# Optimization experiments

Hardware: AMD Instinct MI355X
Metric: run time of the kernel (lower is better)

## Reference

```python
import jax, jax.numpy as jnp
import numpy as np

B, S, HID = 2, 2048, 2048
H, HKV, D = 16, 8, 128
CHUNK = 512
THETA = 1000000.0
NEG = -1e9


def setup_inputs() -> dict:
    key = jax.random.key(0)
    ks = jax.random.split(key, 10)
    hidden_states = jax.random.normal(ks[0], (B, S, HID), dtype=jnp.float32)
    # additive causal mask (0 on/below diagonal, -1e9 above)
    tri = jnp.tril(jnp.ones((S, S), dtype=bool))
    attention_mask = jnp.where(tri, 0.0, NEG).astype(jnp.float32)
    attention_mask = jnp.broadcast_to(attention_mask[None, None], (B, 1, S, S))
    w = 0.02
    Wq = jax.random.normal(ks[1], (HID, H * D), dtype=jnp.float32) * w
    bq = jax.random.normal(ks[2], (H * D,), dtype=jnp.float32) * w
    Wk = jax.random.normal(ks[3], (HID, HKV * D), dtype=jnp.float32) * w
    bk = jax.random.normal(ks[4], (HKV * D,), dtype=jnp.float32) * w
    Wv = jax.random.normal(ks[5], (HID, HKV * D), dtype=jnp.float32) * w
    bv = jax.random.normal(ks[6], (HKV * D,), dtype=jnp.float32) * w
    Wo = jax.random.normal(ks[7], (H * D, HID), dtype=jnp.float32) * w
    bo = jax.random.normal(ks[8], (HID,), dtype=jnp.float32) * w
    return {"hidden_states": hidden_states, "attention_mask": attention_mask,
            "Wq": Wq, "bq": bq, "Wk": Wk, "bk": bk, "Wv": Wv, "bv": bv,
            "Wo": Wo, "bo": bo}


def _rope_tables(seq_len, dim):
    inv_freq = 1.0 / (THETA ** (jnp.arange(0, dim, 2, dtype=jnp.float32) / dim))
    pos = jnp.arange(seq_len, dtype=jnp.float32)
    freqs = pos[:, None] * inv_freq[None, :]          # [S, D/2]
    emb = jnp.concatenate([freqs, freqs], axis=-1)    # [S, D]
    return jnp.cos(emb)[None, None], jnp.sin(emb)[None, None]  # [1,1,S,D]


def _rotate_half(x):
    x1, x2 = jnp.split(x, 2, axis=-1)
    return jnp.concatenate([-x2, x1], axis=-1)


def _attn_forward(hidden_states, attention_mask, Wq, bq, Wk, bk, Wv, bv, Wo, bo):
    bsz, s, _ = hidden_states.shape
    q = (hidden_states @ Wq + bq).reshape(bsz, s, H, D).transpose(0, 2, 1, 3)
    k = (hidden_states @ Wk + bk).reshape(bsz, s, HKV, D).transpose(0, 2, 1, 3)
    v = (hidden_states @ Wv + bv).reshape(bsz, s, HKV, D).transpose(0, 2, 1, 3)
    cos, sin = _rope_tables(s, D)
    q = q * cos + _rotate_half(q) * sin
    k = k * cos + _rotate_half(k) * sin
    n_rep = H // HKV
    k = jnp.repeat(k, n_rep, axis=1)  # repeat_kv
    v = jnp.repeat(v, n_rep, axis=1)
    scale = 1.0 / jnp.sqrt(jnp.float32(D))
    nq, nk = s // CHUNK, s // CHUNK
    Qc = q.reshape(bsz, H, nq, CHUNK, D)
    Kc = jnp.moveaxis(k.reshape(bsz, H, nk, CHUNK, D), 2, 0)   # [nk,B,H,Ck,D]
    Vc = jnp.moveaxis(v.reshape(bsz, H, nk, CHUNK, D), 2, 0)
    Mc = jnp.moveaxis(attention_mask.reshape(bsz, 1, nq, CHUNK, nk, CHUNK), 4, 0)  # [nk,B,1,nq,Cq,Ck]

    def step(carry, xs):
        o, m, d = carry
        k_seg, v_seg, m_seg = xs
        # scores: [B,H,nq,Cq,Ck]
        sc = jnp.einsum('bhqcd,bhkd->bhqck', Qc, k_seg) * scale + m_seg
        new_m = jnp.maximum(m, sc.max(axis=-1, keepdims=True))
        e = jnp.exp(sc - new_m)
        sums = e.sum(axis=-1, keepdims=True)
        prev = jnp.exp(m - new_m)          # NOTE: uses running max, as in source
        d_new = prev + sums
        o = (o * prev + jnp.einsum('bhqck,bhkd->bhqcd', e, v_seg)) / d_new
        return (o, new_m, d_new), None

    o0 = jnp.zeros((bsz, H, nq, CHUNK, D), dtype=jnp.float32)
    m0 = jnp.full((bsz, H, nq, CHUNK, 1), -jnp.inf, dtype=jnp.float32)
    d0 = jnp.ones((bsz, H, nq, CHUNK, 1), dtype=jnp.float32)
    (o, m, d), _ = jax.lax.scan(step, (o0, m0, d0), (Kc, Vc, Mc))
    # final rescale: attn_output * exp(max - logsumexp) == o / d_last (source math)
    o = o / d
    attn = o.reshape(bsz, H, s, D).transpose(0, 2, 1, 3).reshape(bsz, s, H * D)
    return attn @ Wo + bo


def reference(hidden_states, attention_mask, Wq, bq, Wk, bk, Wv, bv, Wo, bo):
    return _attn_forward(hidden_states, attention_mask, Wq, bq, Wk, bk, Wv, bv, Wo, bo)
```

## Files before the change

### kernel.cpp

```cpp
#include <hip/hip_runtime.h>
#include <hip/hip_bf16.h>


typedef __attribute__((ext_vector_type(8))) short s8v;
typedef __attribute__((ext_vector_type(4))) float f4v;

#define MFMA16(a, b, c) __builtin_amdgcn_mfma_f32_16x16x32_bf16((a), (b), (c), 0, 0, 0)

typedef unsigned short u16;
typedef const __attribute__((address_space(1))) unsigned int* gas_p;
typedef __attribute__((address_space(3))) unsigned int* las_p;

__device__ __forceinline__ void gl_lds16(const void* g, void* l) {
    __builtin_amdgcn_global_load_lds((gas_p)g, (las_p)l, 16, 0, 0);
}

__device__ __forceinline__ u16 f2b(float f) {
    __hip_bfloat16 h = __float2bfloat16(f);
    return *reinterpret_cast<u16*>(&h);
}
__device__ __forceinline__ float b2f(u16 u) {
    __hip_bfloat16 h;
    *reinterpret_cast<u16*>(&h) = u;
    return __bfloat162float(h);
}

__device__ const unsigned char qt_tab[80] = {
    8, 9, 10, 11, 12, 13, 14, 15,
    16, 16, 17, 17, 18, 18, 19, 19, 20, 20, 21, 21, 22, 22, 23, 23,
    24, 24, 24, 25, 25, 25, 26, 26, 26, 27, 27, 27,
    28, 28, 28, 29, 29, 29, 30, 30, 30, 31, 31, 31,
    31, 23, 15, 7, 30, 22, 14, 6, 29, 21, 13, 5, 28, 20, 12, 4,
    27, 19, 11, 3, 26, 18, 10, 2, 25, 17, 9, 1, 24, 16, 8, 0};
__device__ const unsigned char c_tab[80] = {
    0, 0, 0, 0, 0, 0, 0, 0,
    0, 1, 0, 1, 0, 1, 0, 1, 0, 1, 0, 1, 0, 1, 0, 1,
    0, 1, 2, 0, 1, 2, 0, 1, 2, 0, 1, 2,
    0, 1, 2, 0, 1, 2, 0, 1, 2, 0, 1, 2,
    3, 2, 1, 0, 3, 2, 1, 0, 3, 2, 1, 0, 3, 2, 1, 0,
    3, 2, 1, 0, 3, 2, 1, 0, 3, 2, 1, 0, 3, 2, 1, 0};

__device__ __forceinline__ int uoff(int qt, int c) {
    int qc = qt >> 3;
    if (c < qc) {
        if (qt < 16) return qt - 8;
        if (qt < 24) return 8 + ((qt - 16) << 1) + c;
        return 24 + (qt - 24) * 3 + c;
    }
    return 48 + ((7 - (qt & 7)) << 2) + (3 - qc);
}

__global__ __launch_bounds__(256) void k_cast_hs(const float* __restrict__ src,
                                                 u16* __restrict__ dst) {
    int i = blockIdx.x * 256 + threadIdx.x;
    float4 v = reinterpret_cast<const float4*>(src)[i];
    alignas(8) u16 t[4] = {f2b(v.x), f2b(v.y), f2b(v.z), f2b(v.w)};
    reinterpret_cast<uint2*>(dst)[i] = *reinterpret_cast<uint2*>(t);
}

__global__ __launch_bounds__(256) void k_transpose_w(
    const float* __restrict__ Wq, const float* __restrict__ Wk,
    const float* __restrict__ Wv, const float* __restrict__ Wo,
    u16* __restrict__ wt_all, u16* __restrict__ wo_t) {
    int id = blockIdx.x;
    const float* W; u16* dst; int N, nbase;
    if (id < 4096)      { W = Wq; dst = wt_all; N = 2048; nbase = 0; }
    else if (id < 6144) { W = Wk; dst = wt_all; N = 1024; nbase = 2048; id -= 4096; }
    else if (id < 8192) { W = Wv; dst = wt_all; N = 1024; nbase = 3072; id -= 6144; }
    else                { W = Wo; dst = wo_t;  N = 2048; nbase = 0;    id -= 8192; }
    int tiles_n = N >> 5;
    int k0 = (id / tiles_n) << 5, n0 = (id % tiles_n) << 5;
    __shared__ float t[32][33];
    int tid = threadIdx.x, c = tid & 31, rr = tid >> 5;
#pragma unroll
    for (int i = 0; i < 4; i++) {
        int kk = rr + i * 8;
        t[kk][c] = W[(size_t)(k0 + kk) * N + n0 + c];
    }
    __syncthreads();
#pragma unroll
    for (int i = 0; i < 4; i++) {
        int n = rr + i * 8;
        dst[(size_t)(nbase + n0 + n) * 2048 + k0 + c] = f2b(t[c][n]);
    }
}

__global__ __launch_bounds__(256) void k_bias(const float* __restrict__ bq,
                                              const float* __restrict__ bk,
                                              const float* __restrict__ bv,
                                              float* __restrict__ dst) {
    int i = blockIdx.x * 256 + threadIdx.x;
    float v = (i < 2048) ? bq[i] : (i < 3072) ? bk[i - 2048] : bv[i - 3072];
    dst[i] = v;
}

__global__ __launch_bounds__(256) void k_gemm(
    const u16* __restrict__ A, const u16* __restrict__ Bt,
    const float* __restrict__ bias, void* __restrict__ out,
    int M, int N, int K, int out_f32) {
    __shared__ alignas(16) u16 As[128][32];
    __shared__ alignas(16) u16 Bs[128][32];
    int tid = threadIdx.x;
    int wave = tid >> 6, lane = tid & 63, quad = lane >> 4, l16 = lane & 15;
    int m0 = blockIdx.y << 7, n0 = blockIdx.x << 7;
    int wm = (wave >> 1) << 6, wn = (wave & 1) << 6;
    f4v zero = {0.f, 0.f, 0.f, 0.f};
    f4v acc[4][4];
#pragma unroll
    for (int a = 0; a < 4; a++)
#pragma unroll
        for (int b = 0; b < 4; b++) acc[a][b] = zero;
    int r0 = tid >> 2;
    int gsw = (tid & 3) ^ ((r0 >> 1) & 3);
    const u16* gA = A + (size_t)(m0 + r0) * K + (gsw << 3);
    const u16* gB = Bt + (size_t)(n0 + r0) * K + (gsw << 3);
    int rg = (quad ^ ((l16 >> 1) & 3)) << 3;
    for (int k0 = 0; k0 < K; k0 += 32) {
        __syncthreads();
#pragma unroll
        for (int i = 0; i < 2; i++) {
            gl_lds16(gA + (size_t)(i << 6) * K + k0, (char*)As + (i << 12) + tid * 16);
            gl_lds16(gB + (size_t)(i << 6) * K + k0, (char*)Bs + (i << 12) + tid * 16);
        }
        __syncthreads();
        s8v af[4], bf_[4];
#pragma unroll
        for (int mi = 0; mi < 4; mi++)
            af[mi] = *reinterpret_cast<const s8v*>(&As[wm + mi * 16 + l16][rg]);
#pragma unroll
        for (int ni = 0; ni < 4; ni++)
            bf_[ni] = *reinterpret_cast<const s8v*>(&Bs[wn + ni * 16 + l16][rg]);
#pragma unroll
        for (int mi = 0; mi < 4; mi++)
#pragma unroll
            for (int ni = 0; ni < 4; ni++)
                acc[mi][ni] = MFMA16(af[mi], bf_[ni], acc[mi][ni]);
    }
#pragma unroll
    for (int mi = 0; mi < 4; mi++) {
#pragma unroll
        for (int ni = 0; ni < 4; ni++) {
            int n = n0 + wn + ni * 16 + l16;
            float bsv = bias[n];
#pragma unroll
            for (int r = 0; r < 4; r++) {
                int m = m0 + wm + mi * 16 + (quad << 2) + r;
                float v = acc[mi][ni][r] + bsv;
                if (out_f32)
                    reinterpret_cast<float*>(out)[(size_t)m * N + n] = v;
                else
                    reinterpret_cast<u16*>(out)[(size_t)m * N + n] = f2b(v);
            }
        }
    }
}

__global__ __launch_bounds__(256) void k_rope(const u16* __restrict__ qkv,
                                              u16* __restrict__ qr,
                                              u16* __restrict__ kr) {
    const float qscale = 0.08838834764831845f * 1.44269504088896340f;
    int row = blockIdx.x;
    int b = row >> 11, s = row & 2047;
    const u16* src = qkv + (size_t)row * 4096;
    __shared__ float lcs[64], lsn[64];
    int tid = threadIdx.x;
    if (tid < 64) {
        float fr = (float)s * exp2f((float)tid * -0.31143075889569023f);
        lcs[tid] = cosf(fr);
        lsn[tid] = sinf(fr);
    }
    __syncthreads();
    for (int u = tid; u < 1536; u += 256) {
        int hh, i;
        const u16* sp;
        u16* dp;
        float sc;
        if (u < 1024) {
            hh = u >> 6; i = u & 63;
            sp = src + hh * 128;
            dp = qr + ((size_t)(b * 16 + hh) * 2048 + s) * 128;
            sc = qscale;
        } else {
            int u2 = u - 1024;
            hh = u2 >> 6; i = u2 & 63;
            sp = src + 2048 + hh * 128;
            dp = kr + ((size_t)(b * 8 + hh) * 2048 + s) * 128;
            sc = 1.f;
        }
        float x1 = b2f(sp[i]);
        float x2 = b2f(sp[i + 64]);
        float cs = lcs[i], sn = lsn[i];
        dp[i]      = f2b((x1 * cs - x2 * sn) * sc);
        dp[i + 64] = f2b((x2 * cs + x1 * sn) * sc);
    }
}

__global__ __launch_bounds__(256) void k_vtrans(const u16* __restrict__ qkv,
                                                u16* __restrict__ vt) {
    int bkv = blockIdx.z, b = bkv >> 3, kv = bkv & 7;
    int s0 = blockIdx.x << 6, d0 = blockIdx.y << 5;
    __shared__ alignas(16) u16 t[32][72];
    int tid = threadIdx.x, c = tid & 31, rr = tid >> 5;
#pragma unroll
    for (int i = 0; i < 8; i++) {
        int s = s0 + rr + i * 8;
        t[c][rr + i * 8] = qkv[(size_t)(b * 2048 + s) * 4096 + 3072 + kv * 128 + d0 + c];
    }
    __syncthreads();
    int dd = tid >> 3, sc8 = (tid & 7) << 3;
    *reinterpret_cast<uint4*>(&vt[((size_t)(b * 8 + kv) * 128 + d0 + dd) * 2048 + s0 + sc8]) =
        *reinterpret_cast<const uint4*>(&t[dd][sc8]);
}

__global__ __launch_bounds__(256) void k_attn_part(const u16* __restrict__ qr,
                                                   const u16* __restrict__ kr,
                                                   const u16* __restrict__ vt,
                                                   u16* __restrict__ PVp,
                                                   float* __restrict__ scp) {
    const float NINF = -__builtin_inff();
    __shared__ alignas(16) u16 Ks[2][64 * 128];
    __shared__ alignas(16) u16 Vs[2][128 * 64];
    __shared__ alignas(16) u16 Pb[4][16][40];

    int tid = threadIdx.x;
    int wv = tid >> 6, lane = tid & 63, quad = lane >> 4, l16 = lane & 15;
    int x = blockIdx.x, h = blockIdx.y, b = blockIdx.z, kvh = h >> 1;
    int qt = qt_tab[x], c = c_tab[x], qc = qt >> 3;
    int nt = (c < qc) ? 8 : (qt & 7) + 1;
    int diagT = (c == qc) ? (qt & 7) : 8;
    int kbase = c << 9;
    const u16* Qp = qr + ((size_t)(b * 16 + h) * 2048 + qt * 64 + wv * 16) * 128;
    const u16* Kp = kr + ((size_t)(b * 8 + kvh) * 2048) * 128;
    const u16* Vp = vt + ((size_t)(b * 8 + kvh) * 128) * 2048;

    s8v qf[4];
#pragma unroll
    for (int sl = 0; sl < 4; sl++)
        qf[sl] = *reinterpret_cast<const s8v*>(&Qp[l16 * 128 + sl * 32 + (quad << 3)]);
    s8v ones;
#pragma unroll
    for (int i = 0; i < 8; i++) ones[i] = (short)0x3F80;

    int krow = tid >> 4, kg = (tid & 15) ^ krow;
    int vd = tid >> 3, vg = (tid & 7) ^ (vd & 7);
    auto stage = [&](int t) {
        int kbt = kbase + (t << 6);
        const u16* kgp = Kp + (size_t)(kbt + krow) * 128 + (kg << 3);
        const u16* vgp = Vp + (size_t)vd * 2048 + kbt + (vg << 3);
        char* kd = (char*)&Ks[t & 1][0];
        char* vdst = (char*)&Vs[t & 1][0];
#pragma unroll
        for (int i = 0; i < 4; i++) {
            gl_lds16(kgp + (size_t)(i << 4) * 128, kd + (i << 12) + tid * 16);
            gl_lds16(vgp + (size_t)(i << 5) * 2048, vdst + (i << 12) + tid * 16);
        }
    };

    f4v zero = {0.f, 0.f, 0.f, 0.f};
    f4v u[8], sums = zero;
#pragma unroll
    for (int ni = 0; ni < 8; ni++) u[ni] = zero;
    float tmx[4] = {NINF, NINF, NINF, NINF};

    stage(0);
    for (int t = 0; t < nt; t++) {
        __syncthreads();
        if (t + 1 < nt) stage(t + 1);
        const char* Kbuf = (const char*)&Ks[t & 1][0];
        const char* Vbuf = (const char*)&Vs[t & 1][0];

        int subs = (t == diagT) ? (wv + 1) : 4;
        int ns2 = (subs + 1) >> 1;
#pragma unroll
        for (int s2 = 0; s2 < 2; s2++) {
            if (s2 >= ns2) continue;
#pragma unroll
            for (int half = 0; half < 2; half++) {
                int sub = (s2 << 1) + half;
                if (sub >= subs) {
#pragma unroll
                    for (int r = 0; r < 4; r++)
                        Pb[wv][(quad << 2) + r][(half << 4) + l16] = (u16)0;
                    continue;
                }
                f4v s = zero;
#pragma unroll
                for (int sl = 0; sl < 4; sl++) {
                    s8v kf = *reinterpret_cast<const s8v*>(
                        Kbuf + ((sub << 4) + l16) * 256 + ((((sl << 2) + quad) ^ l16) << 4));
                    s = MFMA16(qf[sl], kf, s);
                }
                bool part = (t == diagT) && (sub == wv);
#pragma unroll
                for (int r = 0; r < 4; r++) {
                    float v = s[r];
                    if (part && (l16 > (quad << 2) + r)) v = NINF;
                    tmx[r] = fmaxf(tmx[r], v);
                    float e = __builtin_amdgcn_exp2f(v);
                    Pb[wv][(quad << 2) + r][(half << 4) + l16] = f2b(e);
                }
            }
            s8v pf = *reinterpret_cast<const s8v*>(&Pb[wv][l16][quad << 3]);
            sums = MFMA16(pf, ones, sums);
#pragma unroll
            for (int ni = 0; ni < 8; ni++) {
                s8v vf = *reinterpret_cast<const s8v*>(
                    Vbuf + ((ni << 4) + l16) * 128 + ((((s2 << 2) + quad) ^ (l16 & 7)) << 4));
                u[ni] = MFMA16(pf, vf, u[ni]);
            }
        }
    }
#pragma unroll
    for (int r = 0; r < 4; r++)
#pragma unroll
        for (int off = 1; off < 16; off <<= 1)
            tmx[r] = fmaxf(tmx[r], __shfl_xor(tmx[r], off));
    float resc[4];
#pragma unroll
    for (int r = 0; r < 4; r++) resc[r] = __builtin_amdgcn_exp2f(-tmx[r]);

    int slot = (b * 16 + h) * 80 + x;
    u16* pvdst = PVp + (size_t)slot * 8192;
#pragma unroll
    for (int ni = 0; ni < 8; ni++)
#pragma unroll
        for (int r = 0; r < 4; r++)
            pvdst[(wv * 16 + (quad << 2) + r) * 128 + ni * 16 + l16] =
                f2b(u[ni][r] * resc[r]);
    if (l16 == 0) {
        float* scd = scp + (size_t)slot * 128 + wv * 16 + (quad << 2);
#pragma unroll
        for (int r = 0; r < 4; r++) {
            scd[r] = tmx[r] * 0.6931471805599453f;
            scd[64 + r] = sums[r] * resc[r];
        }
    }
}

__global__ __launch_bounds__(256) void k_attn_comb(const u16* __restrict__ PVp,
                                                   const float* __restrict__ scp,
                                                   u16* __restrict__ attnb) {
    int qt = blockIdx.x, h = blockIdx.y, b = blockIdx.z, qc = qt >> 3;
    int tid = threadIdx.x, row = tid >> 2, d0 = (tid & 3) << 5;
    int bh = b * 16 + h;
    float o[32];
#pragma unroll
    for (int i = 0; i < 32; i++) o[i] = 0.f;
    float mprev = -__builtin_inff(), dlast = 1.f;
    for (int cc = 0; cc <= qc; cc++) {
        int slot = bh * 80 + uoff(qt, cc);
        float ch = scp[(size_t)slot * 128 + row];
        float sh = scp[(size_t)slot * 128 + 64 + row];
        float mnew = fmaxf(mprev, ch);
        float p = __expf(mprev - mnew);
        float lam = __expf(ch - mnew);
        float dd = p + lam * sh;
        float inv = 1.f / dd;
        const u16* pv = PVp + (size_t)slot * 8192 + row * 128 + d0;
#pragma unroll
        for (int k = 0; k < 4; k++) {
            s8v v8 = *reinterpret_cast<const s8v*>(pv + (k << 3));
#pragma unroll
            for (int j = 0; j < 8; j++) {
                int i = (k << 3) + j;
                o[i] = (o[i] * p + lam * b2f((u16)v8[j])) * inv;
            }
        }
        mprev = mnew;
        dlast = dd;
    }
    if (qc == 3) {
        float inv = 1.f / dlast;
#pragma unroll
        for (int i = 0; i < 32; i++) o[i] *= inv;
    }
    alignas(16) u16 ob[32];
#pragma unroll
    for (int i = 0; i < 32; i++) ob[i] = f2b(o[i]);
    u16* dst = attnb + (size_t)(b * 2048 + qt * 64 + row) * 2048 + h * 128 + d0;
#pragma unroll
    for (int k = 0; k < 4; k++)
        reinterpret_cast<uint4*>(dst)[k] = reinterpret_cast<const uint4*>(ob)[k];
}

extern "C" void kernel_launch(void* const* d_in, const int* in_sizes, int n_in,
                              void* d_out, int out_size, void* d_ws, size_t ws_size,
                              hipStream_t stream) {
    (void)in_sizes; (void)n_in; (void)out_size; (void)ws_size;
    const float* hs = (const float*)d_in[0];
    const float* Wq = (const float*)d_in[2];
    const float* bq = (const float*)d_in[3];
    const float* Wk = (const float*)d_in[4];
    const float* bk = (const float*)d_in[5];
    const float* Wv = (const float*)d_in[6];
    const float* bv = (const float*)d_in[7];
    const float* Wo = (const float*)d_in[8];
    const float* bo = (const float*)d_in[9];

    char* ws = (char*)d_ws;
    u16* hsb      = (u16*)(ws);
    u16* qr       = hsb;
    u16* attnb    = hsb;
    u16* wt_all   = (u16*)(ws + (16u << 20));
    u16* kr       = wt_all;
    u16* vt       = (u16*)(ws + (24u << 20));
    u16* wo_t     = (u16*)(ws + (32u << 20));
    float* bias_c = (float*)(ws + (40u << 20));
    u16* qkv      = (u16*)(ws + (40u << 20) + 65536);
    u16* PVp      = qkv;
    float* scp    = (float*)(ws + (40u << 20) + 65536 + 41943040u);

    k_cast_hs<<<8192, 256, 0, stream>>>(hs, hsb);
    k_transpose_w<<<12288, 256, 0, stream>>>(Wq, Wk, Wv, Wo, wt_all, wo_t);
    k_bias<<<16, 256, 0, stream>>>(bq, bk, bv, bias_c);
    k_gemm<<<dim3(32, 32), 256, 0, stream>>>(hsb, wt_all, bias_c, qkv,
                                             4096, 4096, 2048, 0);
    k_rope<<<4096, 256, 0, stream>>>(qkv, qr, kr);
    k_vtrans<<<dim3(32, 4, 16), 256, 0, stream>>>(qkv, vt);
    k_attn_part<<<dim3(80, 16, 2), 256, 0, stream>>>(qr, kr, vt, PVp, scp);
    k_attn_comb<<<dim3(32, 16, 2), 256, 0, stream>>>(PVp, scp, attnb);
    k_gemm<<<dim3(16, 32), 256, 0, stream>>>(attnb, wo_t, bo, d_out,
                                             4096, 2048, 2048, 1);
}
```

Baseline: 430.9 us.

## Double attention query tile per wave, deepen GEMM K-step, vectorize weight transpose

```diff
diff --git a/kernel.cpp b/kernel.cpp
--- a/kernel.cpp
+++ b/kernel.cpp
@@ -25,29 +25,25 @@
     return __bfloat162float(h);
 }
 
-__device__ const unsigned char qt_tab[80] = {
-    8, 9, 10, 11, 12, 13, 14, 15,
-    16, 16, 17, 17, 18, 18, 19, 19, 20, 20, 21, 21, 22, 22, 23, 23,
-    24, 24, 24, 25, 25, 25, 26, 26, 26, 27, 27, 27,
-    28, 28, 28, 29, 29, 29, 30, 30, 30, 31, 31, 31,
-    31, 23, 15, 7, 30, 22, 14, 6, 29, 21, 13, 5, 28, 20, 12, 4,
-    27, 19, 11, 3, 26, 18, 10, 2, 25, 17, 9, 1, 24, 16, 8, 0};
-__device__ const unsigned char c_tab[80] = {
-    0, 0, 0, 0, 0, 0, 0, 0,
-    0, 1, 0, 1, 0, 1, 0, 1, 0, 1, 0, 1, 0, 1, 0, 1,
+__device__ const unsigned char qt_tab[40] = {
+    4, 5, 6, 7,
+    8, 8, 9, 9, 10, 10, 11, 11,
+    12, 12, 12, 13, 13, 13, 14, 14, 14, 15, 15, 15,
+    3, 7, 11, 15, 2, 6, 10, 14, 1, 5, 9, 13, 0, 4, 8, 12};
+__device__ const unsigned char c_tab[40] = {
+    0, 0, 0, 0,
+    0, 1, 0, 1, 0, 1, 0, 1,
     0, 1, 2, 0, 1, 2, 0, 1, 2, 0, 1, 2,
-    0, 1, 2, 0, 1, 2, 0, 1, 2, 0, 1, 2,
-    3, 2, 1, 0, 3, 2, 1, 0, 3, 2, 1, 0, 3, 2, 1, 0,
-    3, 2, 1, 0, 3, 2, 1, 0, 3, 2, 1, 0, 3, 2, 1, 0};
-
-__device__ __forceinline__ int uoff(int qt, int c) {
-    int qc = qt >> 3;
+    0, 1, 2, 3, 0, 1, 2, 3, 0, 1, 2, 3, 0, 1, 2, 3};
+
+__device__ __forceinline__ int uoff40(int qt, int c) {
+    int qc = qt >> 2;
     if (c < qc) {
-        if (qt < 16) return qt - 8;
-        if (qt < 24) return 8 + ((qt - 16) << 1) + c;
-        return 24 + (qt - 24) * 3 + c;
-    }
-    return 48 + ((7 - (qt & 7)) << 2) + (3 - qc);
+        if (qt < 8) return qt - 4;
+        if (qt < 12) return 4 + ((qt - 8) << 1) + c;
+        return 12 + (qt - 12) * 3 + c;
+    }
+    return 24 + ((3 - (qt & 3)) << 2) + qc;
 }
 
 __global__ __launch_bounds__(256) void k_cast_hs(const float* __restrict__ src,
@@ -71,17 +67,21 @@
     int tiles_n = N >> 5;
     int k0 = (id / tiles_n) << 5, n0 = (id % tiles_n) << 5;
     __shared__ float t[32][33];
-    int tid = threadIdx.x, c = tid & 31, rr = tid >> 5;
-#pragma unroll
-    for (int i = 0; i < 4; i++) {
-        int kk = rr + i * 8;
-        t[kk][c] = W[(size_t)(k0 + kk) * N + n0 + c];
+    int tid = threadIdx.x;
+    {
+        int row = tid >> 3, c4 = (tid & 7) << 2;
+        float4 v = *reinterpret_cast<const float4*>(&W[(size_t)(k0 + row) * N + n0 + c4]);
+        t[row][c4 + 0] = v.x; t[row][c4 + 1] = v.y;
+        t[row][c4 + 2] = v.z; t[row][c4 + 3] = v.w;
     }
     __syncthreads();
-#pragma unroll
-    for (int i = 0; i < 4; i++) {
-        int n = rr + i * 8;
-        dst[(size_t)(nbase + n0 + n) * 2048 + k0 + c] = f2b(t[c][n]);
+    {
+        int n = tid >> 3, kq = (tid & 7) << 2;
+        alignas(8) u16 p[4];
+#pragma unroll
+        for (int j = 0; j < 4; j++) p[j] = f2b(t[kq + j][n]);
+        *reinterpret_cast<uint2*>(&dst[(size_t)(nbase + n0 + n) * 2048 + k0 + kq]) =
+            *reinterpret_cast<uint2*>(p);
     }
 }
 
@@ -98,8 +98,8 @@
     const u16* __restrict__ A, const u16* __restrict__ Bt,
     const float* __restrict__ bias, void* __restrict__ out,
     int M, int N, int K, int out_f32) {
-    __shared__ alignas(16) u16 As[128][32];
-    __shared__ alignas(16) u16 Bs[128][32];
+    __shared__ alignas(16) u16 As[128][64];
+    __shared__ alignas(16) u16 Bs[128][64];
     int tid = threadIdx.x;
     int wave = tid >> 6, lane = tid & 63, quad = lane >> 4, l16 = lane & 15;
     int m0 = blockIdx.y << 7, n0 = blockIdx.x << 7;
@@ -110,31 +110,34 @@
     for (int a = 0; a < 4; a++)
 #pragma unroll
         for (int b = 0; b < 4; b++) acc[a][b] = zero;
-    int r0 = tid >> 2;
-    int gsw = (tid & 3) ^ ((r0 >> 1) & 3);
+    int r0 = tid >> 3;
+    int gsw = (tid & 7) ^ (r0 & 7);
     const u16* gA = A + (size_t)(m0 + r0) * K + (gsw << 3);
     const u16* gB = Bt + (size_t)(n0 + r0) * K + (gsw << 3);
-    int rg = (quad ^ ((l16 >> 1) & 3)) << 3;
-    for (int k0 = 0; k0 < K; k0 += 32) {
+    for (int k0 = 0; k0 < K; k0 += 64) {
         __syncthreads();
 #pragma unroll
-        for (int i = 0; i < 2; i++) {
-            gl_lds16(gA + (size_t)(i << 6) * K + k0, (char*)As + (i << 12) + tid * 16);
-            gl_lds16(gB + (size_t)(i << 6) * K + k0, (char*)Bs + (i << 12) + tid * 16);
+        for (int i = 0; i < 4; i++) {
+            gl_lds16(gA + (size_t)(i << 5) * K + k0, (char*)As + (i << 12) + tid * 16);
+            gl_lds16(gB + (size_t)(i << 5) * K + k0, (char*)Bs + (i << 12) + tid * 16);
         }
         __syncthreads();
-        s8v af[4], bf_[4];
-#pragma unroll
-        for (int mi = 0; mi < 4; mi++)
-            af[mi] = *reinterpret_cast<const s8v*>(&As[wm + mi * 16 + l16][rg]);
-#pragma unroll
-        for (int ni = 0; ni < 4; ni++)
-            bf_[ni] = *reinterpret_cast<const s8v*>(&Bs[wn + ni * 16 + l16][rg]);
-#pragma unroll
-        for (int mi = 0; mi < 4; mi++)
+#pragma unroll
+        for (int ks = 0; ks < 2; ks++) {
+            int rg = (((ks << 2) | quad) ^ (l16 & 7)) << 3;
+            s8v af[4], bf_[4];
+#pragma unroll
+            for (int mi = 0; mi < 4; mi++)
+                af[mi] = *reinterpret_cast<const s8v*>(&As[wm + mi * 16 + l16][rg]);
 #pragma unroll
             for (int ni = 0; ni < 4; ni++)
-                acc[mi][ni] = MFMA16(af[mi], bf_[ni], acc[mi][ni]);
+                bf_[ni] = *reinterpret_cast<const s8v*>(&Bs[wn + ni * 16 + l16][rg]);
+#pragma unroll
+            for (int mi = 0; mi < 4; mi++)
+#pragma unroll
+                for (int ni = 0; ni < 4; ni++)
+                    acc[mi][ni] = MFMA16(af[mi], bf_[ni], acc[mi][ni]);
+        }
     }
 #pragma unroll
     for (int mi = 0; mi < 4; mi++) {
@@ -220,23 +223,26 @@
     const float NINF = -__builtin_inff();
     __shared__ alignas(16) u16 Ks[2][64 * 128];
     __shared__ alignas(16) u16 Vs[2][128 * 64];
-    __shared__ alignas(16) u16 Pb[4][16][40];
+    __shared__ alignas(16) u16 Pb[4][2][16][40];
 
     int tid = threadIdx.x;
     int wv = tid >> 6, lane = tid & 63, quad = lane >> 4, l16 = lane & 15;
     int x = blockIdx.x, h = blockIdx.y, b = blockIdx.z, kvh = h >> 1;
-    int qt = qt_tab[x], c = c_tab[x], qc = qt >> 3;
-    int nt = (c < qc) ? 8 : (qt & 7) + 1;
-    int diagT = (c == qc) ? (qt & 7) : 8;
+    int qt = qt_tab[x], c = c_tab[x], qc = qt >> 2;
+    bool diag = (c == qc);
+    int m3 = qt & 3;
+    int nt = diag ? ((m3 + 1) << 1) : 8;
     int kbase = c << 9;
-    const u16* Qp = qr + ((size_t)(b * 16 + h) * 2048 + qt * 64 + wv * 16) * 128;
+    const u16* Qp = qr + ((size_t)(b * 16 + h) * 2048 + qt * 128 + wv * 32) * 128;
     const u16* Kp = kr + ((size_t)(b * 8 + kvh) * 2048) * 128;
     const u16* Vp = vt + ((size_t)(b * 8 + kvh) * 128) * 2048;
 
-    s8v qf[4];
-#pragma unroll
-    for (int sl = 0; sl < 4; sl++)
-        qf[sl] = *reinterpret_cast<const s8v*>(&Qp[l16 * 128 + sl * 32 + (quad << 3)]);
+    s8v qf0[4], qf1[4];
+#pragma unroll
+    for (int sl = 0; sl < 4; sl++) {
+        qf0[sl] = *reinterpret_cast<const s8v*>(&Qp[l16 * 128 + sl * 32 + (quad << 3)]);
+        qf1[sl] = *reinterpret_cast<const s8v*>(&Qp[(16 + l16) * 128 + sl * 32 + (quad << 3)]);
+    }
     s8v ones;
 #pragma unroll
     for (int i = 0; i < 8; i++) ones[i] = (short)0x3F80;
@@ -257,10 +263,12 @@
     };
 
     f4v zero = {0.f, 0.f, 0.f, 0.f};
-    f4v u[8], sums = zero;
-#pragma unroll
-    for (int ni = 0; ni < 8; ni++) u[ni] = zero;
-    float tmx[4] = {NINF, NINF, NINF, NINF};
+    f4v u0[8], u1[8], sums0 = zero, sums1 = zero;
+#pragma unroll
+    for (int ni = 0; ni < 8; ni++) { u0[ni] = zero; u1[ni] = zero; }
+    float tmx0[4] = {NINF, NINF, NINF, NINF};
+    float tmx1[4] = {NINF, NINF, NINF, NINF};
+    int qg0 = wv << 1, qg1 = (wv << 1) + 1;
 
     stage(0);
     for (int t = 0; t < nt; t++) {
@@ -268,71 +276,110 @@
         if (t + 1 < nt) stage(t + 1);
         const char* Kbuf = (const char*)&Ks[t & 1][0];
         const char* Vbuf = (const char*)&Vs[t & 1][0];
-
-        int subs = (t == diagT) ? (wv + 1) : 4;
-        int ns2 = (subs + 1) >> 1;
+        int kgb = diag ? ((t << 2) - (m3 << 3)) : -1000;
+
 #pragma unroll
         for (int s2 = 0; s2 < 2; s2++) {
-            if (s2 >= ns2) continue;
+            if (kgb + (s2 << 1) > qg1) continue;
+            bool h0act = (kgb + (s2 << 1) <= qg0);
 #pragma unroll
             for (int half = 0; half < 2; half++) {
                 int sub = (s2 << 1) + half;
-                if (sub >= subs) {
+                int kgi = kgb + sub;
+                if (kgi > qg1) {
+                    if (h0act)
+#pragma unroll
+                        for (int r = 0; r < 4; r++)
+                            Pb[wv][0][(quad << 2) + r][(half << 4) + l16] = (u16)0;
 #pragma unroll
                     for (int r = 0; r < 4; r++)
-                        Pb[wv][(quad << 2) + r][(half << 4) + l16] = (u16)0;
+                        Pb[wv][1][(quad << 2) + r][(half << 4) + l16] = (u16)0;
                     continue;
                 }
-                f4v s = zero;
+                bool act0 = (kgi <= qg0);
+                f4v s0 = zero, s1 = zero;
 #pragma unroll
                 for (int sl = 0; sl < 4; sl++) {
                     s8v kf = *reinterpret_cast<const s8v*>(
                         Kbuf + ((sub << 4) + l16) * 256 + ((((sl << 2) + quad) ^ l16) << 4));
-                    s = MFMA16(qf[sl], kf, s);
+                    if (act0) s0 = MFMA16(qf0[sl], kf, s0);
+                    s1 = MFMA16(qf1[sl], kf, s1);
                 }
-                bool part = (t == diagT) && (sub == wv);
-#pragma unroll
-                for (int r = 0; r < 4; r++) {
-                    float v = s[r];
-                    if (part && (l16 > (quad << 2) + r)) v = NINF;
-                    tmx[r] = fmaxf(tmx[r], v);
-                    float e = __builtin_amdgcn_exp2f(v);
-                    Pb[wv][(quad << 2) + r][(half << 4) + l16] = f2b(e);
+                if (act0) {
+                    bool tri = (kgi == qg0);
+#pragma unroll
+                    for (int r = 0; r < 4; r++) {
+                        float v = s0[r];
+                        if (tri && (l16 > (quad << 2) + r)) v = NINF;
+                        tmx0[r] = fmaxf(tmx0[r], v);
+                        Pb[wv][0][(quad << 2) + r][(half << 4) + l16] =
+                            f2b(__builtin_amdgcn_exp2f(v));
+                    }
+                } else if (h0act) {
+#pragma unroll
+                    for (int r = 0; r < 4; r++)
+                        Pb[wv][0][(quad << 2) + r][(half << 4) + l16] = (u16)0;
+                }
+                {
+                    bool tri = (kgi == qg1);
+#pragma unroll
+                    for (int r = 0; r < 4; r++) {
+                        float v = s1[r];
+                        if (tri && (l16 > (quad << 2) + r)) v = NINF;
+                        tmx1[r] = fmaxf(tmx1[r], v);
+                        Pb[wv][1][(quad << 2) + r][(half << 4) + l16] =
+                            f2b(__builtin_amdgcn_exp2f(v));
+                    }
                 }
             }
-            s8v pf = *reinterpret_cast<const s8v*>(&Pb[wv][l16][quad << 3]);
-            sums = MFMA16(pf, ones, sums);
+            s8v pf0, pf1;
+            if (h0act) {
+                pf0 = *reinterpret_cast<const s8v*>(&Pb[wv][0][l16][quad << 3]);
+                sums0 = MFMA16(pf0, ones, sums0);
+            }
+            pf1 = *reinterpret_cast<const s8v*>(&Pb[wv][1][l16][quad << 3]);
+            sums1 = MFMA16(pf1, ones, sums1);
 #pragma unroll
             for (int ni = 0; ni < 8; ni++) {
                 s8v vf = *reinterpret_cast<const s8v*>(
                     Vbuf + ((ni << 4) + l16) * 128 + ((((s2 << 2) + quad) ^ (l16 & 7)) << 4));
-                u[ni] = MFMA16(pf, vf, u[ni]);
+                if (h0act) u0[ni] = MFMA16(pf0, vf, u0[ni]);
+                u1[ni] = MFMA16(pf1, vf, u1[ni]);
             }
         }
     }
 #pragma unroll
-    for (int r = 0; r < 4; r++)
-#pragma unroll
-        for (int off = 1; off < 16; off <<= 1)
-            tmx[r] = fmaxf(tmx[r], __shfl_xor(tmx[r], off));
-    float resc[4];
-#pragma unroll
-    for (int r = 0; r < 4; r++) resc[r] = __builtin_amdgcn_exp2f(-tmx[r]);
-
-    int slot = (b * 16 + h) * 80 + x;
-    u16* pvdst = PVp + (size_t)slot * 8192;
+    for (int r = 0; r < 4; r++) {
+#pragma unroll
+        for (int off = 1; off < 16; off <<= 1) {
+            tmx0[r] = fmaxf(tmx0[r], __shfl_xor(tmx0[r], off));
+            tmx1[r] = fmaxf(tmx1[r], __shfl_xor(tmx1[r], off));
+        }
+    }
+    float resc0[4], resc1[4];
+#pragma unroll
+    for (int r = 0; r < 4; r++) {
+        resc0[r] = __builtin_amdgcn_exp2f(-tmx0[r]);
+        resc1[r] = __builtin_amdgcn_exp2f(-tmx1[r]);
+    }
+    int slot = (b * 16 + h) * 40 + x;
+    u16* pvdst = PVp + (size_t)slot * 16384;
+    int row0 = wv * 32 + (quad << 2);
 #pragma unroll
     for (int ni = 0; ni < 8; ni++)
 #pragma unroll
-        for (int r = 0; r < 4; r++)
-            pvdst[(wv * 16 + (quad << 2) + r) * 128 + ni * 16 + l16] =
-                f2b(u[ni][r] * resc[r]);
+        for (int r = 0; r < 4; r++) {
+            pvdst[(row0 + r) * 128 + ni * 16 + l16] = f2b(u0[ni][r] * resc0[r]);
+            pvdst[(row0 + 16 + r) * 128 + ni * 16 + l16] = f2b(u1[ni][r] * resc1[r]);
+        }
     if (l16 == 0) {
-        float* scd = scp + (size_t)slot * 128 + wv * 16 + (quad << 2);
+        float* scd = scp + (size_t)slot * 256 + row0;
 #pragma unroll
         for (int r = 0; r < 4; r++) {
-            scd[r] = tmx[r] * 0.6931471805599453f;
-            scd[64 + r] = sums[r] * resc[r];
+            scd[r] = tmx0[r] * 0.6931471805599453f;
+            scd[16 + r] = tmx1[r] * 0.6931471805599453f;
+            scd[128 + r] = sums0[r] * resc0[r];
+            scd[144 + r] = sums1[r] * resc1[r];
         }
     }
 }
@@ -340,23 +387,25 @@
 __global__ __launch_bounds__(256) void k_attn_comb(const u16* __restrict__ PVp,
                                                    const float* __restrict__ scp,
                                                    u16* __restrict__ attnb) {
-    int qt = blockIdx.x, h = blockIdx.y, b = blockIdx.z, qc = qt >> 3;
-    int tid = threadIdx.x, row = tid >> 2, d0 = (tid & 3) << 5;
+    int qt64 = blockIdx.x, h = blockIdx.y, b = blockIdx.z;
+    int qt = qt64 >> 1, qc = qt >> 2;
+    int tid = threadIdx.x;
+    int row = ((qt64 & 1) << 6) + (tid >> 2), d0 = (tid & 3) << 5;
     int bh = b * 16 + h;
     float o[32];
 #pragma unroll
     for (int i = 0; i < 32; i++) o[i] = 0.f;
     float mprev = -__builtin_inff(), dlast = 1.f;
     for (int cc = 0; cc <= qc; cc++) {
-        int slot = bh * 80 + uoff(qt, cc);
-        float ch = scp[(size_t)slot * 128 + row];
-        float sh = scp[(size_t)slot * 128 + 64 + row];
+        int slot = bh * 40 + uoff40(qt, cc);
+        float ch = scp[(size_t)slot * 256 + row];
+        float sh = scp[(size_t)slot * 256 + 128 + row];
         float mnew = fmaxf(mprev, ch);
         float p = __expf(mprev - mnew);
         float lam = __expf(ch - mnew);
         float dd = p + lam * sh;
         float inv = 1.f / dd;
-        const u16* pv = PVp + (size_t)slot * 8192 + row * 128 + d0;
+        const u16* pv = PVp + (size_t)slot * 16384 + row * 128 + d0;
 #pragma unroll
         for (int k = 0; k < 4; k++) {
             s8v v8 = *reinterpret_cast<const s8v*>(pv + (k << 3));
@@ -377,7 +426,7 @@
     alignas(16) u16 ob[32];
 #pragma unroll
     for (int i = 0; i < 32; i++) ob[i] = f2b(o[i]);
-    u16* dst = attnb + (size_t)(b * 2048 + qt * 64 + row) * 2048 + h * 128 + d0;
+    u16* dst = attnb + (size_t)(b * 2048 + qt * 128 + row) * 2048 + h * 128 + d0;
 #pragma unroll
     for (int k = 0; k < 4; k++)
         reinterpret_cast<uint4*>(dst)[k] = reinterpret_cast<const uint4*>(ob)[k];
@@ -417,7 +466,7 @@
                                              4096, 4096, 2048, 0);
     k_rope<<<4096, 256, 0, stream>>>(qkv, qr, kr);
     k_vtrans<<<dim3(32, 4, 16), 256, 0, stream>>>(qkv, vt);
-    k_attn_part<<<dim3(80, 16, 2), 256, 0, stream>>>(qr, kr, vt, PVp, scp);
+    k_attn_part<<<dim3(40, 16, 2), 256, 0, stream>>>(qr, kr, vt, PVp, scp);
     k_attn_comb<<<dim3(32, 16, 2), 256, 0, stream>>>(PVp, scp, attnb);
     k_gemm<<<dim3(16, 32), 256, 0, stream>>>(attnb, wo_t, bo, d_out,
                                              4096, 2048, 2048, 1);
```

After: 412.9 us. 1.04x faster.
